# Optimization experiments

Measured on AMD Instinct MI355X. Metric: run time of the kernel, lower is better.

## Reference

```python
import jax, jax.numpy as jnp
import numpy as np

STATE_LEN = 4096
SEQ_LEN = 8192
T = 1024  # number of time buckets in time_sim_mat


def setup_inputs() -> dict:
    key = jax.random.key(0)
    k1, k2, k3 = jax.random.split(key, 3)
    his = jax.random.randint(k1, (SEQ_LEN,), 0, T, dtype=jnp.int64 if jax.config.jax_enable_x64 else jnp.int32)
    cur = jax.random.randint(k2, (STATE_LEN,), 0, T, dtype=jnp.int64 if jax.config.jax_enable_x64 else jnp.int32)
    time_sim_mat = jax.random.normal(k3, (T, T), dtype=jnp.float32)
    return {"his": his, "cur": cur, "time_sim_mat": time_sim_mat}


def reference(his, cur, time_sim_mat):
    # attn_energies[i, j] = time_sim_mat[cur[i], his[j]]  (vectorized gather)
    energies = time_sim_mat[cur[:, None], his[None, :]]  # [state_len, seq_len]
    return jax.nn.softmax(energies, axis=-1)
```

## Files before the change

### kernel.cpp

```cpp
#include <hip/hip_runtime.h>
#include <cstddef>

#define TDIM 1024
#define SEQ 8192
#define NROWS 4096

typedef float f32x4 __attribute__((ext_vector_type(4)));

__global__ __launch_bounds__(256) void fused_kernel(
    const int* __restrict__ his, const int* __restrict__ cur,
    const float* __restrict__ M, float* __restrict__ out)
{
    __shared__ float mrow[TDIM];
    __shared__ float redm[4];
    __shared__ float reds[4];

    const int tid = threadIdx.x;
    const int row = blockIdx.x;
    const int r = cur[row];
    const float* Mrow = M + (size_t)r * TDIM;

    const int4* his4 = (const int4*)his;
    int4 h[8];
#pragma unroll
    for (int it = 0; it < 8; ++it) h[it] = his4[it * 256 + tid];

#pragma unroll
    for (int k = 0; k < 4; ++k) mrow[tid + 256 * k] = Mrow[tid + 256 * k];
    __syncthreads();

    float g[32];
#pragma unroll
    for (int it = 0; it < 8; ++it) {
        g[4 * it + 0] = mrow[h[it].x];
        g[4 * it + 1] = mrow[h[it].y];
        g[4 * it + 2] = mrow[h[it].z];
        g[4 * it + 3] = mrow[h[it].w];
    }

    float mloc = g[0];
#pragma unroll
    for (int j = 1; j < 32; ++j) mloc = fmaxf(mloc, g[j]);
    float e[32];
    float s = 0.f;
#pragma unroll
    for (int j = 0; j < 32; ++j) {
        e[j] = __expf(g[j] - mloc);
        s += e[j];
    }

    float m = mloc;
#pragma unroll
    for (int off = 32; off > 0; off >>= 1) {
        float om = __shfl_xor(m, off, 64);
        float os = __shfl_xor(s, off, 64);
        float nm_ = fmaxf(m, om);
        s = s * __expf(m - nm_) + os * __expf(om - nm_);
        m = nm_;
    }

    const int wave = tid >> 6, lane = tid & 63;
    if (lane == 0) { redm[wave] = m; reds[wave] = s; }
    __syncthreads();
    float M0 = redm[0], S0 = reds[0];
#pragma unroll
    for (int w = 1; w < 4; ++w) {
        float mw = redm[w], sw = reds[w];
        float nm_ = fmaxf(M0, mw);
        S0 = S0 * __expf(M0 - nm_) + sw * __expf(mw - nm_);
        M0 = nm_;
    }

    const float scale = __expf(mloc - M0) / S0;

    f32x4* out4 = (f32x4*)(out + (size_t)row * SEQ);
#pragma unroll
    for (int it = 0; it < 8; ++it) {
        f32x4 o;
        o.x = e[4 * it + 0] * scale;
        o.y = e[4 * it + 1] * scale;
        o.z = e[4 * it + 2] * scale;
        o.w = e[4 * it + 3] * scale;
        out4[it * 256 + tid] = o;
    }
}

extern "C" void kernel_launch(void* const* d_in, const int* in_sizes, int n_in,
                              void* d_out, int out_size, void* d_ws, size_t ws_size,
                              hipStream_t stream) {
    const int*   his = (const int*)d_in[0];
    const int*   cur = (const int*)d_in[1];
    const float* M   = (const float*)d_in[2];
    float* out = (float*)d_out;
    (void)d_ws; (void)ws_size;

    fused_kernel<<<NROWS, 256, 0, stream>>>(his, cur, M, out);
}
```

Baseline: 143.9 us.

## Compute per-matrix-row softmax stats via histogram, then gather probabilities

Splits the work into two kernels. The first builds a histogram of `his` and computes max and sum-of-exp once for each of the 1024 matrix rows. The second precomputes normalized probabilities for the 1024 entries of the row and gathers them into the output, handling two output rows per block. This removes the per-output-row exp and reduction work across 4096 rows, at the cost of an extra launch, a workspace buffer, and LDS atomics in the stats pass.

```diff
diff --git a/kernel.cpp b/kernel.cpp
--- a/kernel.cpp
+++ b/kernel.cpp
@@ -6,6 +6,112 @@
 #define NROWS 4096
 
 typedef float f32x4 __attribute__((ext_vector_type(4)));
+
+__global__ __launch_bounds__(256) void stats_kernel(
+    const int* __restrict__ his, const float* __restrict__ M,
+    float2* __restrict__ scales)
+{
+    __shared__ int lc[TDIM];
+    __shared__ float red[8];
+    const int tid = threadIdx.x;
+    const int r = blockIdx.x;
+
+#pragma unroll
+    for (int k = 0; k < 4; ++k) lc[tid + 256 * k] = 0;
+
+    const int4* his4 = (const int4*)his;
+    int4 h[8];
+#pragma unroll
+    for (int it = 0; it < 8; ++it) h[it] = his4[it * 256 + tid];
+
+    const float* Mrow = M + (size_t)r * TDIM;
+    float m[4];
+#pragma unroll
+    for (int k = 0; k < 4; ++k) m[k] = Mrow[tid + 256 * k];
+
+    __syncthreads();
+#pragma unroll
+    for (int it = 0; it < 8; ++it) {
+        atomicAdd(&lc[h[it].x], 1);
+        atomicAdd(&lc[h[it].y], 1);
+        atomicAdd(&lc[h[it].z], 1);
+        atomicAdd(&lc[h[it].w], 1);
+    }
+    __syncthreads();
+
+    int c[4];
+#pragma unroll
+    for (int k = 0; k < 4; ++k) c[k] = lc[tid + 256 * k];
+
+    float lmax = -3.402823466e38f;
+#pragma unroll
+    for (int k = 0; k < 4; ++k)
+        if (c[k] > 0) lmax = fmaxf(lmax, m[k]);
+#pragma unroll
+    for (int off = 32; off > 0; off >>= 1)
+        lmax = fmaxf(lmax, __shfl_down(lmax, off, 64));
+    const int wave = tid >> 6, lane = tid & 63;
+    if (lane == 0) red[wave] = lmax;
+    __syncthreads();
+    const float gmax = fmaxf(fmaxf(red[0], red[1]), fmaxf(red[2], red[3]));
+
+    float lsum = 0.f;
+#pragma unroll
+    for (int k = 0; k < 4; ++k)
+        lsum += (float)c[k] * __expf(m[k] - gmax);
+#pragma unroll
+    for (int off = 32; off > 0; off >>= 1)
+        lsum += __shfl_down(lsum, off, 64);
+    if (lane == 0) red[4 + wave] = lsum;
+    __syncthreads();
+    if (tid == 0) {
+        float s = red[4] + red[5] + red[6] + red[7];
+        scales[r] = make_float2(gmax, 1.0f / s);
+    }
+}
+
+__global__ __launch_bounds__(256) void out_kernel(
+    const int* __restrict__ his, const int* __restrict__ cur,
+    const float* __restrict__ M, const float2* __restrict__ scales,
+    float* __restrict__ out)
+{
+    __shared__ float prob[2][TDIM];
+    const int tid = threadIdx.x;
+    const int row0 = blockIdx.x * 2;
+    const int r0 = cur[row0];
+    const int r1 = cur[row0 + 1];
+    const float2 s0 = scales[r0];
+    const float2 s1 = scales[r1];
+    const float* M0 = M + (size_t)r0 * TDIM;
+    const float* M1 = M + (size_t)r1 * TDIM;
+
+    const int4* his4 = (const int4*)his;
+    int4 h[8];
+#pragma unroll
+    for (int it = 0; it < 8; ++it) h[it] = his4[it * 256 + tid];
+
+#pragma unroll
+    for (int k = 0; k < 4; ++k) {
+        int t = tid + 256 * k;
+        prob[0][t] = __expf(M0[t] - s0.x) * s0.y;
+        prob[1][t] = __expf(M1[t] - s1.x) * s1.y;
+    }
+    __syncthreads();
+
+    f32x4* o0 = (f32x4*)(out + (size_t)row0 * SEQ);
+    f32x4* o1 = (f32x4*)(out + (size_t)(row0 + 1) * SEQ);
+#pragma unroll
+    for (int it = 0; it < 8; ++it) {
+        const int4 hh = h[it];
+        f32x4 a, b;
+        a.x = prob[0][hh.x];  b.x = prob[1][hh.x];
+        a.y = prob[0][hh.y];  b.y = prob[1][hh.y];
+        a.z = prob[0][hh.z];  b.z = prob[1][hh.z];
+        a.w = prob[0][hh.w];  b.w = prob[1][hh.w];
+        o0[it * 256 + tid] = a;
+        o1[it * 256 + tid] = b;
+    }
+}
 
 __global__ __launch_bounds__(256) void fused_kernel(
     const int* __restrict__ his, const int* __restrict__ cur,
@@ -92,7 +198,12 @@
     const int*   cur = (const int*)d_in[1];
     const float* M   = (const float*)d_in[2];
     float* out = (float*)d_out;
-    (void)d_ws; (void)ws_size;
-
-    fused_kernel<<<NROWS, 256, 0, stream>>>(his, cur, M, out);
-}
+
+    if (ws_size >= TDIM * sizeof(float2)) {
+        float2* scales = (float2*)d_ws;
+        stats_kernel<<<TDIM, 256, 0, stream>>>(his, M, scales);
+        out_kernel<<<NROWS / 2, 256, 0, stream>>>(his, cur, M, scales, out);
+    } else {
+        fused_kernel<<<NROWS, 256, 0, stream>>>(his, cur, M, out);
+    }
+}
```

After: 144.9 us. About the same (+0.7%).
